# Kernel optimization log

Hardware: AMD Instinct MI355X
Metric: run time of the kernel (lower is better)

## Reference

```python
import jax, jax.numpy as jnp
import numpy as np

LEVELS = 16
FEATURES = 2
TABLE_SIZE = 2 ** 19
MINRES = (16, 16)
MAXRES = (2048, 2048)
N = 2 ** 21  # number of query points
PRIMES = (1, 2654435761)  # Instant-NGP spatial hash primes (2D)


def _level_res():
    # per-dim geometric growth: floor(minres * b**l), b = exp((ln(max)-ln(min))/(L-1))
    res = []
    for l in range(LEVELS):
        r = []
        for mn, mx in zip(MINRES, MAXRES):
            b = np.exp((np.log(mx) - np.log(mn)) / (LEVELS - 1))
            r.append(int(np.floor(mn * b ** l)))
        res.append(tuple(r))
    return res


RES_LEVELS = _level_res()


def setup_inputs() -> dict:
    key = jax.random.key(0)
    k1, k2, k3, k4 = jax.random.split(key, 4)
    coords_x = jax.random.uniform(k1, (N,), jnp.float32)
    coords_y = jax.random.uniform(k2, (N,), jnp.float32)
    # level 0 is a dense grid table; levels 1..L-1 are hash tables (stacked)
    dense_table = jax.random.uniform(k3, (*RES_LEVELS[0], FEATURES), jnp.float32, -1e-4, 1e-4)
    hash_tables = jax.random.uniform(k4, (LEVELS - 1, TABLE_SIZE, FEATURES), jnp.float32, -1e-4, 1e-4)
    return {"coords_x": coords_x, "coords_y": coords_y,
            "dense_table": dense_table, "hash_tables": hash_tables}


def _bilerp(gather, res, cx, cy):
    # normalized coords in [0,1] scaled to index space [0, res-1]; mode='nearest' -> clamp
    rx, ry = res
    fx = cx * (rx - 1)
    fy = cy * (ry - 1)
    x0 = jnp.floor(fx)
    y0 = jnp.floor(fy)
    wx = (fx - x0)[:, None]
    wy = (fy - y0)[:, None]
    ix0 = jnp.clip(x0.astype(jnp.int32), 0, rx - 1)
    iy0 = jnp.clip(y0.astype(jnp.int32), 0, ry - 1)
    ix1 = jnp.minimum(ix0 + 1, rx - 1)
    iy1 = jnp.minimum(iy0 + 1, ry - 1)
    f00 = gather(ix0, iy0)  # [N, F]
    f01 = gather(ix0, iy1)
    f10 = gather(ix1, iy0)
    f11 = gather(ix1, iy1)
    return (f00 * (1 - wx) * (1 - wy) + f01 * (1 - wx) * wy
            + f10 * wx * (1 - wy) + f11 * wx * wy)


def _hash_gather(table, ix, iy):
    h = (ix.astype(jnp.uint32) * jnp.uint32(PRIMES[0])) ^ (iy.astype(jnp.uint32) * jnp.uint32(PRIMES[1]))
    idx = (h % jnp.uint32(table.shape[0])).astype(jnp.int32)
    return table[idx]


def reference(coords_x, coords_y, dense_table, hash_tables):
    feats = [_bilerp(lambda ix, iy: dense_table[ix, iy], RES_LEVELS[0], coords_x, coords_y)]
    for l in range(1, LEVELS):
        t = hash_tables[l - 1]
        feats.append(_bilerp(lambda ix, iy, t=t: _hash_gather(t, ix, iy),
                             RES_LEVELS[l], coords_x, coords_y))
    return jnp.concatenate(feats, -1)  # [N, LEVELS*FEATURES]
```

## Files before the change

kernel.cpp:

```cpp
#include <hip/hip_runtime.h>
#include <math.h>
#include <stdint.h>


#define TMASK  ((1u << 19) - 1)
#define PRIME2 2654435761u
#define NBIN   16384u
#define CAP    192u
#define INVOG  0xFFFFFFFFu

typedef float vfloat4 __attribute__((ext_vector_type(4)));
typedef float vfloat2 __attribute__((ext_vector_type(2)));

__device__ __forceinline__ void pair_gather(const char* tp, unsigned h0,
                                            unsigned h1, float2& a, float2& b)
{
    if (((h0 ^ h1) | 1u) == 1u) {
        vfloat4 q = *(const vfloat4*)(tp + ((h0 & ~1u) << 3));
        a.x = (h0 & 1u) ? q.z : q.x;  a.y = (h0 & 1u) ? q.w : q.y;
        b.x = (h1 & 1u) ? q.z : q.x;  b.y = (h1 & 1u) ? q.w : q.y;
    } else {
        a = *(const float2*)(tp + ((size_t)h0 << 3));
        b = *(const float2*)(tp + ((size_t)h1 << 3));
    }
}

__device__ __forceinline__ unsigned bin_of(float x, float y)
{
    int bx = (int)(x * 128.0f); bx = bx < 0 ? 0 : (bx > 127 ? 127 : bx);
    int by = (int)(y * 128.0f); by = by < 0 ? 0 : (by > 127 ? 127 : by);
    return (unsigned)by * 128u + (unsigned)bx;
}

__global__ void k_init(float* __restrict__ bx, float* __restrict__ by,
                       unsigned* __restrict__ og, unsigned* __restrict__ cnt,
                       unsigned NS)
{
    unsigned i = blockIdx.x * 256u + threadIdx.x;
    if (i < NS) { bx[i] = -1.0f; by[i] = -1.0f; og[i] = INVOG; }
    if (i <= NBIN) cnt[i] = 0u;
}

__global__ void k_scatter(const float* __restrict__ cx, const float* __restrict__ cy,
                          unsigned* __restrict__ cnt, float* __restrict__ bx,
                          float* __restrict__ by, unsigned* __restrict__ og,
                          float* __restrict__ ox, float* __restrict__ oy,
                          unsigned* __restrict__ oidx, unsigned N)
{
    unsigned i = blockIdx.x * 256u + threadIdx.x;
    if (i >= N) return;
    float x = cx[i], y = cy[i];
    unsigned b = bin_of(x, y);
    unsigned pos = atomicAdd(&cnt[b], 1u);
    if (pos < CAP) {
        unsigned s = b * CAP + pos;
        bx[s] = x; by[s] = y; og[s] = i;
    } else {
        unsigned op = atomicAdd(&cnt[NBIN], 1u);
        ox[op] = x; oy[op] = y; oidx[op] = i;
    }
}

__global__ __launch_bounds__(256, 8) void mre_big(
    const float* __restrict__ px, const float* __restrict__ py,
    const float2* __restrict__ hasht, vfloat2* __restrict__ ws,
    uint4 rm1v, unsigned NS)
{
    unsigned bid = blockIdx.x;
    unsigned xcd = bid & 7u;
    unsigned lv  = xcd >> 1;
    unsigned bwl = (bid >> 3) * 2u + (xcd & 1u);
    int r = (int)(lv == 0u ? rm1v.x : lv == 1u ? rm1v.y
                                    : lv == 2u ? rm1v.z : rm1v.w);
    const char* hb = (const char*)hasht + ((size_t)(11u + lv) << 22);
    vfloat2* wbase = ws + (size_t)lv * NS;
    float rf = (float)r;

    unsigned stride = 512u * 256u;
    #pragma unroll 2
    for (unsigned n = bwl * 256u + threadIdx.x; n < NS; n += stride) {
        float x = px[n], y = py[n];
        if (__ballot(x >= 0.0f) == 0ull) continue;
        float fx = x * rf, fy = y * rf;
        float x0f = floorf(fx), y0f = floorf(fy);
        float wx = fx - x0f, wy = fy - y0f;
        int ix0 = (int)x0f; ix0 = ix0 < 0 ? 0 : (ix0 > r ? r : ix0);
        int iy0 = (int)y0f; iy0 = iy0 < 0 ? 0 : (iy0 > r ? r : iy0);
        int ix1 = ix0 + 1 > r ? r : ix0 + 1;
        int iy1 = iy0 + 1 > r ? r : iy0 + 1;
        unsigned hy0 = (unsigned)iy0 * PRIME2;
        unsigned hy1 = (unsigned)iy1 * PRIME2;
        unsigned h00 = ((unsigned)ix0 ^ hy0) & TMASK;
        unsigned h10 = ((unsigned)ix1 ^ hy0) & TMASK;
        unsigned h01 = ((unsigned)ix0 ^ hy1) & TMASK;
        unsigned h11 = ((unsigned)ix1 ^ hy1) & TMASK;
        float2 f00, f01, f10, f11;
        pair_gather(hb, h00, h10, f00, f10);
        pair_gather(hb, h01, h11, f01, f11);
        float omx = 1.0f - wx, omy = 1.0f - wy;
        float w00 = omx * omy, w01 = omx * wy, w10 = wx * omy, w11 = wx * wy;
        vfloat2 acc;
        acc.x = f00.x * w00 + f01.x * w01 + f10.x * w10 + f11.x * w11;
        acc.y = f00.y * w00 + f01.y * w01 + f10.y * w10 + f11.y * w11;
        __builtin_nontemporal_store(acc, wbase + n);
    }
}

__global__ __launch_bounds__(256) void mre_rest_s(
    const float* __restrict__ bx, const float* __restrict__ by,
    const unsigned* __restrict__ og,
    const float2* __restrict__ dense, const float2* __restrict__ hasht,
    const vfloat2* __restrict__ ws, float4* __restrict__ out,
    uint4 wa, uint4 wb, unsigned NS)
{
    __shared__ float2 sdense[256];
    __shared__ __align__(16) float sout[64 * 36];
    __shared__ unsigned sorig[64];
    sdense[threadIdx.x] = dense[threadIdx.x];

    unsigned j  = threadIdx.x >> 6;
    unsigned nl = threadIdx.x & 63u;
    unsigned slot = blockIdx.x * 64u + nl;
    unsigned o = og[slot];
    if (j == 0u) sorig[nl] = o;
    __syncthreads();

    bool valid = (o != INVOG);
    if (__ballot(valid) != 0ull) {
        float x = bx[slot];
        float y = by[slot];
        vfloat2 wsv = __builtin_nontemporal_load(&ws[(size_t)j * NS + slot]);

        unsigned W0 = wa.x, W1 = wa.y, W2 = wa.z, W3 = wa.w, W4 = wb.x, W5 = wb.y;
        unsigned u0 = j == 0u ? W0 : j == 1u ? W1 : j == 2u ? W3 : W4;
        unsigned u1 = j == 0u ? W0 : j == 1u ? W2 : j == 2u ? W3 : W5;
        unsigned u2 = j == 0u ? W1 : j == 1u ? W2 : j == 2u ? W4 : W5;
        unsigned s0 = (j & 1u) << 4;
        unsigned s1 = ((j + 1u) & 1u) << 4;
        int rm1[3] = { (int)((u0 >> s0) & 0xffffu),
                       (int)((u1 >> s1) & 0xffffu),
                       (int)((u2 >> s0) & 0xffffu) };

        unsigned h00[3], h01[3], h10[3], h11[3];
        unsigned tbo[3];
        float wx[3], wy[3];
        unsigned d00 = 0, d01 = 0, d10 = 0, d11 = 0;

        #pragma unroll
        for (int k = 0; k < 3; ++k) {
            int r = rm1[k];
            float rf = (float)r;
            float fx = x * rf, fy = y * rf;
            float x0f = floorf(fx), y0f = floorf(fy);
            wx[k] = fx - x0f;  wy[k] = fy - y0f;
            int ix0 = (int)x0f; ix0 = ix0 < 0 ? 0 : (ix0 > r ? r : ix0);
            int iy0 = (int)y0f; iy0 = iy0 < 0 ? 0 : (iy0 > r ? r : iy0);
            int ix1 = ix0 + 1 > r ? r : ix0 + 1;
            int iy1 = iy0 + 1 > r ? r : iy0 + 1;
            if (k == 0) { d00 = ix0 * 16 + iy0; d01 = ix0 * 16 + iy1;
                          d10 = ix1 * 16 + iy0; d11 = ix1 * 16 + iy1; }
            unsigned lvl = j * 3u + (unsigned)k;
            unsigned ti = lvl == 0u ? 0u : lvl - 1u;
            tbo[k] = ti << 22;
            unsigned hy0 = (unsigned)iy0 * PRIME2;
            unsigned hy1 = (unsigned)iy1 * PRIME2;
            h00[k] = ((unsigned)ix0 ^ hy0) & TMASK;
            h01[k] = ((unsigned)ix0 ^ hy1) & TMASK;
            h10[k] = ((unsigned)ix1 ^ hy0) & TMASK;
            h11[k] = ((unsigned)ix1 ^ hy1) & TMASK;
        }

        const char* hb = (const char*)hasht;
        float2 f00[3], f01[3], f10[3], f11[3];
        #pragma unroll
        for (int k = 1; k < 3; ++k) {
            const char* tp = hb + tbo[k];
            pair_gather(tp, h00[k], h10[k], f00[k], f10[k]);
            pair_gather(tp, h01[k], h11[k], f01[k], f11[k]);
        }
        if (j == 0u) {
            f00[0] = sdense[d00]; f01[0] = sdense[d01];
            f10[0] = sdense[d10]; f11[0] = sdense[d11];
        } else {
            const char* tp = hb + tbo[0];
            pair_gather(tp, h00[0], h10[0], f00[0], f10[0]);
            pair_gather(tp, h01[0], h11[0], f01[0], f11[0]);
        }

        float* so = &sout[nl * 36u];
        #pragma unroll
        for (int k = 0; k < 3; ++k) {
            float omx = 1.0f - wx[k], omy = 1.0f - wy[k];
            float w00 = omx * omy, w01 = omx * wy[k];
            float w10 = wx[k] * omy, w11 = wx[k] * wy[k];
            vfloat2 a;
            a.x = f00[k].x * w00 + f01[k].x * w01 + f10[k].x * w10 + f11[k].x * w11;
            a.y = f00[k].y * w00 + f01[k].y * w01 + f10[k].y * w10 + f11[k].y * w11;
            *(vfloat2*)&so[6u * j + 2u * (unsigned)k] = a;
        }
        *(vfloat2*)&so[24u + 2u * j] = wsv;
    }
    __syncthreads();

    unsigned c  = threadIdx.x & 7u;
    unsigned q0 = threadIdx.x >> 3;
    #pragma unroll
    for (int p = 0; p < 2; ++p) {
        unsigned q = q0 + 32u * p;
        unsigned oo = sorig[q];
        if (oo != INVOG) {
            vfloat4 v = *(const vfloat4*)&sout[q * 36u + c * 4u];
            __builtin_nontemporal_store(v, (vfloat4*)(out + (size_t)oo * 8u + c));
        }
    }
}

__global__ void k_overflow(const float* __restrict__ ox, const float* __restrict__ oy,
                           const unsigned* __restrict__ oidx,
                           const unsigned* __restrict__ cnt,
                           const float2* __restrict__ dense,
                           const float2* __restrict__ hasht,
                           float4* __restrict__ out, uint4 wa, uint4 wb)
{
    unsigned ocnt = cnt[NBIN];
    unsigned pwv[8] = { wa.x, wa.y, wa.z, wa.w, wb.x, wb.y, wb.z, wb.w };
    const char* hb = (const char*)hasht;
    for (unsigned i = blockIdx.x * 256u + threadIdx.x; i < ocnt;
         i += gridDim.x * 256u) {
        float x = ox[i], y = oy[i];
        float f[32];
        #pragma unroll
        for (int l = 0; l < 16; ++l) {
            int r = (int)((pwv[l >> 1] >> ((l & 1) << 4)) & 0xffffu);
            float rf = (float)r;
            float fx = x * rf, fy = y * rf;
            float x0f = floorf(fx), y0f = floorf(fy);
            float wx = fx - x0f, wy = fy - y0f;
            int ix0 = (int)x0f; ix0 = ix0 < 0 ? 0 : (ix0 > r ? r : ix0);
            int iy0 = (int)y0f; iy0 = iy0 < 0 ? 0 : (iy0 > r ? r : iy0);
            int ix1 = ix0 + 1 > r ? r : ix0 + 1;
            int iy1 = iy0 + 1 > r ? r : iy0 + 1;
            float2 f00, f01, f10, f11;
            if (l == 0) {
                f00 = dense[ix0 * 16 + iy0]; f01 = dense[ix0 * 16 + iy1];
                f10 = dense[ix1 * 16 + iy0]; f11 = dense[ix1 * 16 + iy1];
            } else {
                const char* tp = hb + ((size_t)(l - 1) << 22);
                unsigned hy0 = (unsigned)iy0 * PRIME2;
                unsigned hy1 = (unsigned)iy1 * PRIME2;
                f00 = *(const float2*)(tp + ((size_t)(((unsigned)ix0 ^ hy0) & TMASK) << 3));
                f01 = *(const float2*)(tp + ((size_t)(((unsigned)ix0 ^ hy1) & TMASK) << 3));
                f10 = *(const float2*)(tp + ((size_t)(((unsigned)ix1 ^ hy0) & TMASK) << 3));
                f11 = *(const float2*)(tp + ((size_t)(((unsigned)ix1 ^ hy1) & TMASK) << 3));
            }
            float omx = 1.0f - wx, omy = 1.0f - wy;
            float w00 = omx * omy, w01 = omx * wy, w10 = wx * omy, w11 = wx * wy;
            f[2 * l]     = f00.x * w00 + f01.x * w01 + f10.x * w10 + f11.x * w11;
            f[2 * l + 1] = f00.y * w00 + f01.y * w01 + f10.y * w10 + f11.y * w11;
        }
        unsigned o = oidx[i];
        float4* ob = out + (size_t)o * 8u;
        #pragma unroll
        for (int c = 0; c < 8; ++c) {
            vfloat4 v = { f[4 * c], f[4 * c + 1], f[4 * c + 2], f[4 * c + 3] };
            __builtin_nontemporal_store(v, (vfloat4*)&ob[c]);
        }
    }
}

__global__ __launch_bounds__(256) void mre_rest(
    const float* __restrict__ cxp, const float* __restrict__ cyp,
    const float2* __restrict__ dense, const float2* __restrict__ hasht,
    const vfloat2* __restrict__ ws, float4* __restrict__ out,
    uint4 wa, uint4 wb, unsigned N)
{
    __shared__ float2 sdense[256];
    __shared__ __align__(16) float sout[64 * 36];
    sdense[threadIdx.x] = dense[threadIdx.x];
    __syncthreads();

    unsigned gid = blockIdx.x * 256u + threadIdx.x;
    unsigned n  = gid >> 2;
    unsigned j  = gid & 3u;
    unsigned nl = threadIdx.x >> 2;

    float x = cxp[n];
    float y = cyp[n];
    vfloat2 wsv = __builtin_nontemporal_load(&ws[(size_t)j * N + n]);

    unsigned W0 = wa.x, W1 = wa.y, W2 = wa.z, W3 = wa.w, W4 = wb.x, W5 = wb.y;
    unsigned u0 = j == 0u ? W0 : j == 1u ? W1 : j == 2u ? W3 : W4;
    unsigned u1 = j == 0u ? W0 : j == 1u ? W2 : j == 2u ? W3 : W5;
    unsigned u2 = j == 0u ? W1 : j == 1u ? W2 : j == 2u ? W4 : W5;
    unsigned s0 = (j & 1u) << 4;
    unsigned s1 = ((j + 1u) & 1u) << 4;
    int rm1[3] = { (int)((u0 >> s0) & 0xffffu),
                   (int)((u1 >> s1) & 0xffffu),
                   (int)((u2 >> s0) & 0xffffu) };

    unsigned h00[3], h01[3], h10[3], h11[3];
    unsigned tbo[3];
    float wx[3], wy[3];
    unsigned d00 = 0, d01 = 0, d10 = 0, d11 = 0;

    #pragma unroll
    for (int k = 0; k < 3; ++k) {
        int r = rm1[k];
        float rf = (float)r;
        float fx = x * rf, fy = y * rf;
        float x0f = floorf(fx), y0f = floorf(fy);
        wx[k] = fx - x0f;  wy[k] = fy - y0f;
        int ix0 = (int)x0f; ix0 = ix0 < 0 ? 0 : (ix0 > r ? r : ix0);
        int iy0 = (int)y0f; iy0 = iy0 < 0 ? 0 : (iy0 > r ? r : iy0);
        int ix1 = ix0 + 1 > r ? r : ix0 + 1;
        int iy1 = iy0 + 1 > r ? r : iy0 + 1;
        if (k == 0) { d00 = ix0 * 16 + iy0; d01 = ix0 * 16 + iy1;
                      d10 = ix1 * 16 + iy0; d11 = ix1 * 16 + iy1; }
        unsigned lvl = j * 3u + (unsigned)k;
        unsigned ti = lvl == 0u ? 0u : lvl - 1u;
        tbo[k] = ti << 22;
        unsigned hy0 = (unsigned)iy0 * PRIME2;
        unsigned hy1 = (unsigned)iy1 * PRIME2;
        h00[k] = ((unsigned)ix0 ^ hy0) & TMASK;
        h01[k] = ((unsigned)ix0 ^ hy1) & TMASK;
        h10[k] = ((unsigned)ix1 ^ hy0) & TMASK;
        h11[k] = ((unsigned)ix1 ^ hy1) & TMASK;
    }

    const char* hb = (const char*)hasht;
    float2 f00[3], f01[3], f10[3], f11[3];
    #pragma unroll
    for (int k = 1; k < 3; ++k) {
        const char* tp = hb + tbo[k];
        pair_gather(tp, h00[k], h10[k], f00[k], f10[k]);
        pair_gather(tp, h01[k], h11[k], f01[k], f11[k]);
    }
    if (j == 0u) {
        f00[0] = sdense[d00]; f01[0] = sdense[d01];
        f10[0] = sdense[d10]; f11[0] = sdense[d11];
    } else {
        const char* tp = hb + tbo[0];
        pair_gather(tp, h00[0], h10[0], f00[0], f10[0]);
        pair_gather(tp, h01[0], h11[0], f01[0], f11[0]);
    }

    float* so = &sout[nl * 36u];
    #pragma unroll
    for (int k = 0; k < 3; ++k) {
        float omx = 1.0f - wx[k], omy = 1.0f - wy[k];
        float w00 = omx * omy, w01 = omx * wy[k];
        float w10 = wx[k] * omy, w11 = wx[k] * wy[k];
        vfloat2 a;
        a.x = f00[k].x * w00 + f01[k].x * w01 + f10[k].x * w10 + f11[k].x * w11;
        a.y = f00[k].y * w00 + f01[k].y * w01 + f10[k].y * w10 + f11[k].y * w11;
        *(vfloat2*)&so[6u * j + 2u * (unsigned)k] = a;
    }
    *(vfloat2*)&so[24u + 2u * j] = wsv;

    __syncthreads();

    const vfloat4* sp = (const vfloat4*)&sout[nl * 36u + 8u * j];
    vfloat4 o0 = sp[0];
    vfloat4 o1 = sp[1];
    size_t base = (size_t)n * 8u + 2u * j;
    __builtin_nontemporal_store(o0, (vfloat4*)&out[base]);
    __builtin_nontemporal_store(o1, (vfloat4*)&out[base + 1]);
}

__global__ __launch_bounds__(256) void mre_mono(
    const float* __restrict__ cxp, const float* __restrict__ cyp,
    const float2* __restrict__ dense, const float2* __restrict__ hasht,
    float4* __restrict__ out, uint4 wa, uint4 wb)
{
    __shared__ float2 sdense[256];
    sdense[threadIdx.x] = dense[threadIdx.x];
    __syncthreads();

    unsigned gid = blockIdx.x * 256u + threadIdx.x;
    unsigned n = gid >> 2;
    unsigned j = gid & 3u;

    float x = cxp[n];
    float y = cyp[n];

    unsigned w0 = j < 2u ? (j == 0u ? wa.x : wa.z) : (j == 2u ? wb.x : wb.z);
    unsigned w1 = j < 2u ? (j == 0u ? wa.y : wa.w) : (j == 2u ? wb.y : wb.w);
    int rm1[4] = { (int)(w0 & 0xffffu), (int)(w0 >> 16),
                   (int)(w1 & 0xffffu), (int)(w1 >> 16) };

    unsigned o00[4], o01[4], o10[4], o11[4];
    float wx[4], wy[4];
    unsigned d00 = 0, d01 = 0, d10 = 0, d11 = 0;
    const bool lvl0 = (j == 0u);

    #pragma unroll
    for (int k = 0; k < 4; ++k) {
        int r = rm1[k];
        float rf = (float)r;
        float fx = x * rf, fy = y * rf;
        float x0f = floorf(fx), y0f = floorf(fy);
        wx[k] = fx - x0f;  wy[k] = fy - y0f;
        int ix0 = (int)x0f; ix0 = ix0 < 0 ? 0 : (ix0 > r ? r : ix0);
        int iy0 = (int)y0f; iy0 = iy0 < 0 ? 0 : (iy0 > r ? r : iy0);
        int ix1 = ix0 + 1 > r ? r : ix0 + 1;
        int iy1 = iy0 + 1 > r ? r : iy0 + 1;
        if (k == 0) { d00 = ix0 * 16 + iy0; d01 = ix0 * 16 + iy1;
                      d10 = ix1 * 16 + iy0; d11 = ix1 * 16 + iy1; }
        unsigned ti = j * 4u + (unsigned)k;
        ti = ti == 0u ? 0u : ti - 1u;
        unsigned tb = ti << 22;
        unsigned hy0 = (unsigned)iy0 * PRIME2;
        unsigned hy1 = (unsigned)iy1 * PRIME2;
        o00[k] = tb + ((((unsigned)ix0 ^ hy0) & TMASK) << 3);
        o01[k] = tb + ((((unsigned)ix0 ^ hy1) & TMASK) << 3);
        o10[k] = tb + ((((unsigned)ix1 ^ hy0) & TMASK) << 3);
        o11[k] = tb + ((((unsigned)ix1 ^ hy1) & TMASK) << 3);
    }

    const char* hb = (const char*)hasht;
    float2 f00[4], f01[4], f10[4], f11[4];
    #pragma unroll
    for (int k = 1; k < 4; ++k) {
        f00[k] = *(const float2*)(hb + o00[k]);
        f01[k] = *(const float2*)(hb + o01[k]);
        f10[k] = *(const float2*)(hb + o10[k]);
        f11[k] = *(const float2*)(hb + o11[k]);
    }
    if (lvl0) {
        f00[0] = sdense[d00]; f01[0] = sdense[d01];
        f10[0] = sdense[d10]; f11[0] = sdense[d11];
    } else {
        f00[0] = *(const float2*)(hb + o00[0]);
        f01[0] = *(const float2*)(hb + o01[0]);
        f10[0] = *(const float2*)(hb + o10[0]);
        f11[0] = *(const float2*)(hb + o11[0]);
    }

    float2 acc[4];
    #pragma unroll
    for (int k = 0; k < 4; ++k) {
        float omx = 1.0f - wx[k], omy = 1.0f - wy[k];
        float w00 = omx * omy, w01 = omx * wy[k];
        float w10 = wx[k] * omy, w11 = wx[k] * wy[k];
        acc[k].x = f00[k].x * w00 + f01[k].x * w01 + f10[k].x * w10 + f11[k].x * w11;
        acc[k].y = f00[k].y * w00 + f01[k].y * w01 + f10[k].y * w10 + f11[k].y * w11;
    }

    vfloat4 o0 = { acc[0].x, acc[0].y, acc[1].x, acc[1].y };
    vfloat4 o1 = { acc[2].x, acc[2].y, acc[3].x, acc[3].y };
    size_t base = (size_t)n * 8u + 2u * j;
    __builtin_nontemporal_store(o0, (vfloat4*)&out[base]);
    __builtin_nontemporal_store(o1, (vfloat4*)&out[base + 1]);
}

extern "C" void kernel_launch(void* const* d_in, const int* in_sizes, int n_in,
                              void* d_out, int out_size, void* d_ws, size_t ws_size,
                              hipStream_t stream)
{
    const float*  cx    = (const float*)d_in[0];
    const float*  cy    = (const float*)d_in[1];
    const float2* dense = (const float2*)d_in[2];
    const float2* hasht = (const float2*)d_in[3];
    float4*       out   = (float4*)d_out;
    const unsigned N = (unsigned)in_sizes[0];

    int r[16];
    for (int l = 0; l < 16; ++l) {
        double b = exp((log(2048.0) - log(16.0)) / 15.0);
        r[l] = (int)floor(16.0 * pow(b, (double)l));
    }
    unsigned pw[8];
    for (int k = 0; k < 8; ++k)
        pw[k] = (unsigned)(r[2 * k] - 1) | ((unsigned)(r[2 * k + 1] - 1) << 16);
    uint4 wa = make_uint4(pw[0], pw[1], pw[2], pw[3]);
    uint4 wb = make_uint4(pw[4], pw[5], pw[6], pw[7]);
    uint4 rm1v = make_uint4((unsigned)(r[12] - 1), (unsigned)(r[13] - 1),
                            (unsigned)(r[14] - 1), (unsigned)(r[15] - 1));

    long long total = (long long)N * 4;
    int blocks  = (int)((total + 255) / 256);
    int pblocks = (int)((N + 255u) / 256u);

    const unsigned NS = NBIN * CAP;
    size_t tbl_bytes    = (size_t)N * 32u;
    size_t sorted_bytes = (size_t)NS * 32u
                        + (size_t)NS * 12u
                        + (size_t)(NBIN + 1) * 4u
                        + (size_t)N * 12u;

    if (ws_size >= sorted_bytes && d_ws != nullptr) {
        char* p = (char*)d_ws;
        vfloat2*  wst = (vfloat2*)p;        p += (size_t)NS * 32u;
        float*    bx  = (float*)p;          p += (size_t)NS * 4u;
        float*    by  = (float*)p;          p += (size_t)NS * 4u;
        unsigned* og  = (unsigned*)p;       p += (size_t)NS * 4u;
        unsigned* cnt = (unsigned*)p;       p += (size_t)(NBIN + 1) * 4u;
        float*    ox  = (float*)p;          p += (size_t)N * 4u;
        float*    oy  = (float*)p;          p += (size_t)N * 4u;
        unsigned* oix = (unsigned*)p;

        int iblocks = (int)((NS + 255u) / 256u);
        hipLaunchKernelGGL(k_init,    dim3(iblocks), dim3(256), 0, stream,
                           bx, by, og, cnt, NS);
        hipLaunchKernelGGL(k_scatter, dim3(pblocks), dim3(256), 0, stream,
                           cx, cy, cnt, bx, by, og, ox, oy, oix, N);
        hipLaunchKernelGGL(mre_big,   dim3(2048), dim3(256), 0, stream,
                           bx, by, hasht, wst, rm1v, NS);
        hipLaunchKernelGGL(mre_rest_s, dim3(NS / 64u), dim3(256), 0, stream,
                           bx, by, og, dense, hasht, (const vfloat2*)wst,
                           out, wa, wb, NS);
        hipLaunchKernelGGL(k_overflow, dim3(64), dim3(256), 0, stream,
                           ox, oy, oix, cnt, dense, hasht, out, wa, wb);
    } else if (ws_size >= tbl_bytes && d_ws != nullptr) {
        vfloat2* wst = (vfloat2*)d_ws;
        hipLaunchKernelGGL(mre_big, dim3(2048), dim3(256), 0, stream,
                           cx, cy, hasht, wst, rm1v, N);
        hipLaunchKernelGGL(mre_rest, dim3(blocks), dim3(256), 0, stream,
                           cx, cy, dense, hasht, (const vfloat2*)wst,
                           out, wa, wb, N);
    } else {
        hipLaunchKernelGGL(mre_mono, dim3(blocks), dim3(256), 0, stream,
                           cx, cy, dense, hasht, out, wa, wb);
    }
}
```

Measured before the change: 666.1 us.

## Fuse big-level pass into spatially sorted kernel and pack slot records

Drops the separate mre_big pass over the binned slots. Each of the four warps per point group in the sorted kernel now computes four levels instead of three, so all 16 levels run in a single kernel after binning. Slot x, y and the original index are packed into one 16-byte record, which also serves as the validity flag. This removes the intermediate workspace write and read plus one launch. The cost is that the largest hash levels are now gathered in the sorted kernel, with more registers per thread, instead of being spread across XCDs by level.

```diff
diff --git a/kernel.cpp b/kernel.cpp
--- a/kernel.cpp
+++ b/kernel.cpp
@@ -32,18 +32,16 @@
     return (unsigned)by * 128u + (unsigned)bx;
 }
 
-__global__ void k_init(float* __restrict__ bx, float* __restrict__ by,
-                       unsigned* __restrict__ og, unsigned* __restrict__ cnt,
+__global__ void k_init(vfloat4* __restrict__ slots, unsigned* __restrict__ cnt,
                        unsigned NS)
 {
     unsigned i = blockIdx.x * 256u + threadIdx.x;
-    if (i < NS) { bx[i] = -1.0f; by[i] = -1.0f; og[i] = INVOG; }
+    if (i < NS) { vfloat4 s = { -1.0f, -1.0f, 0.0f, 0.0f }; slots[i] = s; }
     if (i <= NBIN) cnt[i] = 0u;
 }
 
 __global__ void k_scatter(const float* __restrict__ cx, const float* __restrict__ cy,
-                          unsigned* __restrict__ cnt, float* __restrict__ bx,
-                          float* __restrict__ by, unsigned* __restrict__ og,
+                          unsigned* __restrict__ cnt, vfloat4* __restrict__ slots,
                           float* __restrict__ ox, float* __restrict__ oy,
                           unsigned* __restrict__ oidx, unsigned N)
 {
@@ -53,65 +51,18 @@
     unsigned b = bin_of(x, y);
     unsigned pos = atomicAdd(&cnt[b], 1u);
     if (pos < CAP) {
-        unsigned s = b * CAP + pos;
-        bx[s] = x; by[s] = y; og[s] = i;
+        vfloat4 rec = { x, y, __uint_as_float(i), 0.0f };
+        slots[b * CAP + pos] = rec;
     } else {
         unsigned op = atomicAdd(&cnt[NBIN], 1u);
         ox[op] = x; oy[op] = y; oidx[op] = i;
     }
 }
 
-__global__ __launch_bounds__(256, 8) void mre_big(
-    const float* __restrict__ px, const float* __restrict__ py,
-    const float2* __restrict__ hasht, vfloat2* __restrict__ ws,
-    uint4 rm1v, unsigned NS)
-{
-    unsigned bid = blockIdx.x;
-    unsigned xcd = bid & 7u;
-    unsigned lv  = xcd >> 1;
-    unsigned bwl = (bid >> 3) * 2u + (xcd & 1u);
-    int r = (int)(lv == 0u ? rm1v.x : lv == 1u ? rm1v.y
-                                    : lv == 2u ? rm1v.z : rm1v.w);
-    const char* hb = (const char*)hasht + ((size_t)(11u + lv) << 22);
-    vfloat2* wbase = ws + (size_t)lv * NS;
-    float rf = (float)r;
-
-    unsigned stride = 512u * 256u;
-    #pragma unroll 2
-    for (unsigned n = bwl * 256u + threadIdx.x; n < NS; n += stride) {
-        float x = px[n], y = py[n];
-        if (__ballot(x >= 0.0f) == 0ull) continue;
-        float fx = x * rf, fy = y * rf;
-        float x0f = floorf(fx), y0f = floorf(fy);
-        float wx = fx - x0f, wy = fy - y0f;
-        int ix0 = (int)x0f; ix0 = ix0 < 0 ? 0 : (ix0 > r ? r : ix0);
-        int iy0 = (int)y0f; iy0 = iy0 < 0 ? 0 : (iy0 > r ? r : iy0);
-        int ix1 = ix0 + 1 > r ? r : ix0 + 1;
-        int iy1 = iy0 + 1 > r ? r : iy0 + 1;
-        unsigned hy0 = (unsigned)iy0 * PRIME2;
-        unsigned hy1 = (unsigned)iy1 * PRIME2;
-        unsigned h00 = ((unsigned)ix0 ^ hy0) & TMASK;
-        unsigned h10 = ((unsigned)ix1 ^ hy0) & TMASK;
-        unsigned h01 = ((unsigned)ix0 ^ hy1) & TMASK;
-        unsigned h11 = ((unsigned)ix1 ^ hy1) & TMASK;
-        float2 f00, f01, f10, f11;
-        pair_gather(hb, h00, h10, f00, f10);
-        pair_gather(hb, h01, h11, f01, f11);
-        float omx = 1.0f - wx, omy = 1.0f - wy;
-        float w00 = omx * omy, w01 = omx * wy, w10 = wx * omy, w11 = wx * wy;
-        vfloat2 acc;
-        acc.x = f00.x * w00 + f01.x * w01 + f10.x * w10 + f11.x * w11;
-        acc.y = f00.y * w00 + f01.y * w01 + f10.y * w10 + f11.y * w11;
-        __builtin_nontemporal_store(acc, wbase + n);
-    }
-}
-
-__global__ __launch_bounds__(256) void mre_rest_s(
-    const float* __restrict__ bx, const float* __restrict__ by,
-    const unsigned* __restrict__ og,
+__global__ __launch_bounds__(256) void mre_all(
+    const vfloat4* __restrict__ slots,
     const float2* __restrict__ dense, const float2* __restrict__ hasht,
-    const vfloat2* __restrict__ ws, float4* __restrict__ out,
-    uint4 wa, uint4 wb, unsigned NS)
+    float4* __restrict__ out, uint4 wa, uint4 wb)
 {
     __shared__ float2 sdense[256];
     __shared__ __align__(16) float sout[64 * 36];
@@ -121,33 +72,25 @@
     unsigned j  = threadIdx.x >> 6;
     unsigned nl = threadIdx.x & 63u;
     unsigned slot = blockIdx.x * 64u + nl;
-    unsigned o = og[slot];
-    if (j == 0u) sorig[nl] = o;
+    vfloat4 rec = slots[slot];
+    float x = rec.x, y = rec.y;
+    bool valid = (x >= 0.0f);
+    if (j == 0u) sorig[nl] = valid ? __float_as_uint(rec.z) : INVOG;
     __syncthreads();
 
-    bool valid = (o != INVOG);
     if (__ballot(valid) != 0ull) {
-        float x = bx[slot];
-        float y = by[slot];
-        vfloat2 wsv = __builtin_nontemporal_load(&ws[(size_t)j * NS + slot]);
-
-        unsigned W0 = wa.x, W1 = wa.y, W2 = wa.z, W3 = wa.w, W4 = wb.x, W5 = wb.y;
-        unsigned u0 = j == 0u ? W0 : j == 1u ? W1 : j == 2u ? W3 : W4;
-        unsigned u1 = j == 0u ? W0 : j == 1u ? W2 : j == 2u ? W3 : W5;
-        unsigned u2 = j == 0u ? W1 : j == 1u ? W2 : j == 2u ? W4 : W5;
-        unsigned s0 = (j & 1u) << 4;
-        unsigned s1 = ((j + 1u) & 1u) << 4;
-        int rm1[3] = { (int)((u0 >> s0) & 0xffffu),
-                       (int)((u1 >> s1) & 0xffffu),
-                       (int)((u2 >> s0) & 0xffffu) };
-
-        unsigned h00[3], h01[3], h10[3], h11[3];
-        unsigned tbo[3];
-        float wx[3], wy[3];
+        unsigned w0 = j == 0u ? wa.x : j == 1u ? wa.z : j == 2u ? wb.x : wb.z;
+        unsigned w1 = j == 0u ? wa.y : j == 1u ? wa.w : j == 2u ? wb.y : wb.w;
+        int rm1[4] = { (int)(w0 & 0xffffu), (int)(w0 >> 16),
+                       (int)(w1 & 0xffffu), (int)(w1 >> 16) };
+
+        unsigned h00[4], h01[4], h10[4], h11[4];
+        unsigned tbo[4];
+        float wx[4], wy[4];
         unsigned d00 = 0, d01 = 0, d10 = 0, d11 = 0;
 
         #pragma unroll
-        for (int k = 0; k < 3; ++k) {
+        for (int k = 0; k < 4; ++k) {
             int r = rm1[k];
             float rf = (float)r;
             float fx = x * rf, fy = y * rf;
@@ -159,7 +102,7 @@
             int iy1 = iy0 + 1 > r ? r : iy0 + 1;
             if (k == 0) { d00 = ix0 * 16 + iy0; d01 = ix0 * 16 + iy1;
                           d10 = ix1 * 16 + iy0; d11 = ix1 * 16 + iy1; }
-            unsigned lvl = j * 3u + (unsigned)k;
+            unsigned lvl = j * 4u + (unsigned)k;
             unsigned ti = lvl == 0u ? 0u : lvl - 1u;
             tbo[k] = ti << 22;
             unsigned hy0 = (unsigned)iy0 * PRIME2;
@@ -171,9 +114,9 @@
         }
 
         const char* hb = (const char*)hasht;
-        float2 f00[3], f01[3], f10[3], f11[3];
+        float2 f00[4], f01[4], f10[4], f11[4];
         #pragma unroll
-        for (int k = 1; k < 3; ++k) {
+        for (int k = 1; k < 4; ++k) {
             const char* tp = hb + tbo[k];
             pair_gather(tp, h00[k], h10[k], f00[k], f10[k]);
             pair_gather(tp, h01[k], h11[k], f01[k], f11[k]);
@@ -187,18 +130,17 @@
             pair_gather(tp, h01[0], h11[0], f01[0], f11[0]);
         }
 
-        float* so = &sout[nl * 36u];
+        float* so = &sout[nl * 36u + 8u * j];
         #pragma unroll
-        for (int k = 0; k < 3; ++k) {
+        for (int k = 0; k < 4; ++k) {
             float omx = 1.0f - wx[k], omy = 1.0f - wy[k];
             float w00 = omx * omy, w01 = omx * wy[k];
             float w10 = wx[k] * omy, w11 = wx[k] * wy[k];
             vfloat2 a;
             a.x = f00[k].x * w00 + f01[k].x * w01 + f10[k].x * w10 + f11[k].x * w11;
             a.y = f00[k].y * w00 + f01[k].y * w01 + f10[k].y * w10 + f11[k].y * w11;
-            *(vfloat2*)&so[6u * j + 2u * (unsigned)k] = a;
-        }
-        *(vfloat2*)&so[24u + 2u * j] = wsv;
+            *(vfloat2*)&so[2u * (unsigned)k] = a;
+        }
     }
     __syncthreads();
 
@@ -268,6 +210,50 @@
     }
 }
 
+__global__ __launch_bounds__(256, 8) void mre_big(
+    const float* __restrict__ px, const float* __restrict__ py,
+    const float2* __restrict__ hasht, vfloat2* __restrict__ ws,
+    uint4 rm1v, unsigned N)
+{
+    unsigned bid = blockIdx.x;
+    unsigned xcd = bid & 7u;
+    unsigned lv  = xcd >> 1;
+    unsigned bwl = (bid >> 3) * 2u + (xcd & 1u);
+    int r = (int)(lv == 0u ? rm1v.x : lv == 1u ? rm1v.y
+                                    : lv == 2u ? rm1v.z : rm1v.w);
+    const char* hb = (const char*)hasht + ((size_t)(11u + lv) << 22);
+    vfloat2* wbase = ws + (size_t)lv * N;
+    float rf = (float)r;
+
+    unsigned stride = 512u * 256u;
+    #pragma unroll 2
+    for (unsigned n = bwl * 256u + threadIdx.x; n < N; n += stride) {
+        float x = px[n], y = py[n];
+        float fx = x * rf, fy = y * rf;
+        float x0f = floorf(fx), y0f = floorf(fy);
+        float wx = fx - x0f, wy = fy - y0f;
+        int ix0 = (int)x0f; ix0 = ix0 < 0 ? 0 : (ix0 > r ? r : ix0);
+        int iy0 = (int)y0f; iy0 = iy0 < 0 ? 0 : (iy0 > r ? r : iy0);
+        int ix1 = ix0 + 1 > r ? r : ix0 + 1;
+        int iy1 = iy0 + 1 > r ? r : iy0 + 1;
+        unsigned hy0 = (unsigned)iy0 * PRIME2;
+        unsigned hy1 = (unsigned)iy1 * PRIME2;
+        unsigned h00 = ((unsigned)ix0 ^ hy0) & TMASK;
+        unsigned h10 = ((unsigned)ix1 ^ hy0) & TMASK;
+        unsigned h01 = ((unsigned)ix0 ^ hy1) & TMASK;
+        unsigned h11 = ((unsigned)ix1 ^ hy1) & TMASK;
+        float2 f00, f01, f10, f11;
+        pair_gather(hb, h00, h10, f00, f10);
+        pair_gather(hb, h01, h11, f01, f11);
+        float omx = 1.0f - wx, omy = 1.0f - wy;
+        float w00 = omx * omy, w01 = omx * wy, w10 = wx * omy, w11 = wx * wy;
+        vfloat2 acc;
+        acc.x = f00.x * w00 + f01.x * w01 + f10.x * w10 + f11.x * w11;
+        acc.y = f00.y * w00 + f01.y * w01 + f10.y * w10 + f11.y * w11;
+        __builtin_nontemporal_store(acc, wbase + n);
+    }
+}
+
 __global__ __launch_bounds__(256) void mre_rest(
     const float* __restrict__ cxp, const float* __restrict__ cyp,
     const float2* __restrict__ dense, const float2* __restrict__ hasht,
@@ -483,32 +469,25 @@
 
     const unsigned NS = NBIN * CAP;
     size_t tbl_bytes    = (size_t)N * 32u;
-    size_t sorted_bytes = (size_t)NS * 32u
-                        + (size_t)NS * 12u
+    size_t sorted_bytes = (size_t)NS * 16u
                         + (size_t)(NBIN + 1) * 4u
                         + (size_t)N * 12u;
 
     if (ws_size >= sorted_bytes && d_ws != nullptr) {
         char* p = (char*)d_ws;
-        vfloat2*  wst = (vfloat2*)p;        p += (size_t)NS * 32u;
-        float*    bx  = (float*)p;          p += (size_t)NS * 4u;
-        float*    by  = (float*)p;          p += (size_t)NS * 4u;
-        unsigned* og  = (unsigned*)p;       p += (size_t)NS * 4u;
-        unsigned* cnt = (unsigned*)p;       p += (size_t)(NBIN + 1) * 4u;
-        float*    ox  = (float*)p;          p += (size_t)N * 4u;
-        float*    oy  = (float*)p;          p += (size_t)N * 4u;
-        unsigned* oix = (unsigned*)p;
+        vfloat4*  slots = (vfloat4*)p;      p += (size_t)NS * 16u;
+        unsigned* cnt   = (unsigned*)p;     p += (size_t)(NBIN + 1) * 4u;
+        float*    ox    = (float*)p;        p += (size_t)N * 4u;
+        float*    oy    = (float*)p;        p += (size_t)N * 4u;
+        unsigned* oix   = (unsigned*)p;
 
         int iblocks = (int)((NS + 255u) / 256u);
         hipLaunchKernelGGL(k_init,    dim3(iblocks), dim3(256), 0, stream,
-                           bx, by, og, cnt, NS);
+                           slots, cnt, NS);
         hipLaunchKernelGGL(k_scatter, dim3(pblocks), dim3(256), 0, stream,
-                           cx, cy, cnt, bx, by, og, ox, oy, oix, N);
-        hipLaunchKernelGGL(mre_big,   dim3(2048), dim3(256), 0, stream,
-                           bx, by, hasht, wst, rm1v, NS);
-        hipLaunchKernelGGL(mre_rest_s, dim3(NS / 64u), dim3(256), 0, stream,
-                           bx, by, og, dense, hasht, (const vfloat2*)wst,
-                           out, wa, wb, NS);
+                           cx, cy, cnt, slots, ox, oy, oix, N);
+        hipLaunchKernelGGL(mre_all,   dim3(NS / 64u), dim3(256), 0, stream,
+                           slots, dense, hasht, out, wa, wb);
         hipLaunchKernelGGL(k_overflow, dim3(64), dim3(256), 0, stream,
                            ox, oy, oix, cnt, dense, hasht, out, wa, wb);
     } else if (ws_size >= tbl_bytes && d_ws != nullptr) {
```

New measurement: 588.7 us. 11.6% less time.
